# Kernel optimization log

Hardware: AMD Instinct MI355X
Metric: run time of the kernel (lower is better)

The kernel has to match this reference:

```python
import jax, jax.numpy as jnp
import numpy as np

P = 8  # patch size hardcoded in FSAS/DFFN
EPS = 1e-5


def conv1x1(x, w):
    # x: [B,C,H,W], w: [Cout,Cin]
    return jnp.einsum('bchw,oc->bohw', x, w)


def dwconv3(x, w):
    # depthwise 3x3, w: [C,1,3,3]
    return jax.lax.conv_general_dilated(
        x, w, window_strides=(1, 1), padding='SAME',
        dimension_numbers=('NCHW', 'OIHW', 'NCHW'),
        feature_group_count=x.shape[1])


def layernorm_c(x, w, b):
    # WithBias LayerNorm over channel dim (torch: b c h w -> b (h w) c, LN over c)
    mu = jnp.mean(x, axis=1, keepdims=True)
    var = jnp.var(x, axis=1, keepdims=True)
    return (x - mu) / jnp.sqrt(var + EPS) * w[None, :, None, None] + b[None, :, None, None]


def to_patches(x):
    # [B,C,H,W] -> [B,C,H/P,W/P,P,P]
    B, C, H, W = x.shape
    return x.reshape(B, C, H // P, P, W // P, P).transpose(0, 1, 2, 4, 3, 5)


def from_patches(xp):
    B, C, h, w, p1, p2 = xp.shape
    return xp.transpose(0, 1, 2, 4, 3, 5).reshape(B, C, h * p1, w * p2)


def fsas(x, w_hidden, dw, norm_w, norm_b, w_out):
    hidden = conv1x1(x, w_hidden)          # [B,6d,H,W]
    qkv = dwconv3(hidden, dw)
    q, k, v = jnp.split(qkv, 3, axis=1)    # each [B,2d,H,W]
    qf = jnp.fft.rfft2(to_patches(q))
    kf = jnp.fft.rfft2(to_patches(k))
    out = jnp.fft.irfft2(qf * kf, s=(P, P))
    out = layernorm_c(from_patches(out), norm_w, norm_b)
    return conv1x1(v * out, w_out)


def dffn(x, w_in, fft_w, dw, w_out):
    x = conv1x1(x, w_in)                   # [B,2h,H,W]
    xf = jnp.fft.rfft2(to_patches(x))
    # fft_w: [2h,1,1,P,P//2+1] broadcasts against [B,2h,h,w,P,P//2+1]
    x = from_patches(jnp.fft.irfft2(xf * fft_w, s=(P, P)))
    x1, x2 = jnp.split(dwconv3(x, dw), 2, axis=1)
    return conv1x1(jax.nn.gelu(x1, approximate=False) * x2, w_out)


def setup_inputs() -> dict:
    key = jax.random.key(0)
    ks = jax.random.split(key, 10)
    d = 48
    h = int(d * 3)  # ffn_expansion_factor=3 -> hidden_features=144
    B, H, W = 2, 256, 256

    def n(k, shape, s=0.05):
        return jax.random.normal(k, shape, jnp.float32) * s

    return {
        'x': jax.random.normal(ks[0], (B, d, H, W), jnp.float32),
        'norm1_w': jnp.ones((d,), jnp.float32),
        'norm1_b': jnp.zeros((d,), jnp.float32),
        'attn_w_hidden': n(ks[1], (6 * d, d)),
        'attn_dw': n(ks[2], (6 * d, 1, 3, 3), 0.2),
        'attn_norm_w': jnp.ones((2 * d,), jnp.float32),
        'attn_norm_b': jnp.zeros((2 * d,), jnp.float32),
        'attn_w_out': n(ks[3], (d, 2 * d)),
        'norm2_w': jnp.ones((d,), jnp.float32),
        'norm2_b': jnp.zeros((d,), jnp.float32),
        'ffn_w_in': n(ks[4], (2 * h, d)),
        'ffn_fft': 1.0 + n(ks[5], (2 * h, 1, 1, P, P // 2 + 1), 0.1),
        'ffn_dw': n(ks[6], (2 * h, 1, 3, 3), 0.2),
        'ffn_w_out': n(ks[7], (d, h)),
    }


def reference(x, norm1_w, norm1_b, attn_w_hidden, attn_dw, attn_norm_w,
              attn_norm_b, attn_w_out, norm2_w, norm2_b, ffn_w_in, ffn_fft,
              ffn_dw, ffn_w_out):
    x = x + fsas(layernorm_c(x, norm1_w, norm1_b),
                 attn_w_hidden, attn_dw, attn_norm_w, attn_norm_b, attn_w_out)
    x = x + dffn(layernorm_c(x, norm2_w, norm2_b),
                 ffn_w_in, ffn_fft, ffn_dw, ffn_w_out)
    return x
```

## Files before the change

kernel.cpp:

```cpp
#include <hip/hip_runtime.h>
#include <hip/hip_bf16.h>
#include <cstddef>


constexpr int HWC = 65536;

typedef short short8 __attribute__((ext_vector_type(8)));
typedef __bf16 bf16x8 __attribute__((ext_vector_type(8)));
typedef float f32x4 __attribute__((ext_vector_type(4)));
typedef _Float16 f16x8 __attribute__((ext_vector_type(8)));
typedef _Float16 f16x4 __attribute__((ext_vector_type(4)));

__device__ inline unsigned short f2bf(float f) {
  __hip_bfloat16 h = __float2bfloat16(f);
  return *reinterpret_cast<unsigned short*>(&h);
}
__device__ inline float bf2f(unsigned short u) {
  __hip_bfloat16 h;
  *reinterpret_cast<unsigned short*>(&h) = u;
  return __bfloat162float(h);
}

union V8 { uint4 v; unsigned short us[8]; short s[8]; };

__device__ inline void load8f(const unsigned short* p, float* f) {
  V8 u; u.v = *reinterpret_cast<const uint4*>(p);
#pragma unroll
  for (int j = 0; j < 8; j++) f[j] = bf2f(u.us[j]);
}
__device__ inline void store8bf(unsigned short* p, const float* f) {
  V8 u;
#pragma unroll
  for (int j = 0; j < 8; j++) u.us[j] = f2bf(f[j]);
  *reinterpret_cast<uint4*>(p) = u.v;
}

__device__ inline void fdft8(const float* x, float* e) {
  const float c = 0.70710678118654752f;
  float t0 = x[0] + x[4], t1 = x[0] - x[4];
  float t2 = x[2] + x[6], t3 = x[2] - x[6];
  float t4 = x[1] + x[5], t5 = x[1] - x[5];
  float t6 = x[3] + x[7], t7 = x[3] - x[7];
  float A = c * (t5 - t7), B = c * (t5 + t7);
  float s1 = t0 + t2, s2 = t4 + t6;
  e[0] = s1 + s2;
  e[7] = s1 - s2;
  e[1] = t1 + A;
  e[5] = t1 - A;
  e[2] = -(B + t3);
  e[6] = t3 - B;
  e[3] = t0 - t2;
  e[4] = t6 - t4;
}

__device__ inline void idft8(const float* Z, float* acc) {
  const float c2 = 0.70710678118654752f;
  float Z0 = Z[0], Z1r = Z[1], Z1i = Z[2], Z2r = Z[3];
  float Z2i = Z[4], Z3r = Z[5], Z3i = Z[6], Z4 = Z[7];
  float u0 = Z0 + Z4, u1 = Z0 - Z4;
  float E = 2.f * Z2r, F = 2.f * (Z1r + Z3r), G = 2.f * (Z1i - Z3i);
  float T = 2.f * Z2i;
  float P = 2.f * c2 * (Z1r - Z1i), Qv = 2.f * c2 * (Z1r + Z1i);
  float R = 2.f * c2 * (Z3r + Z3i), S = 2.f * c2 * (Z3r - Z3i);
  acc[0] = 0.125f * (u0 + E + F);
  acc[4] = 0.125f * (u0 + E - F);
  acc[2] = 0.125f * (u0 - E - G);
  acc[6] = 0.125f * (u0 - E + G);
  acc[1] = 0.125f * (u1 + P - T - R);
  acc[3] = 0.125f * (u1 - Qv + T + S);
  acc[5] = 0.125f * (u1 - P - T + R);
  acc[7] = 0.125f * (u1 + Qv + T - S);
}

__device__ const float c_cos8[8] = {
    1.f, 0.70710678118654752f, 0.f, -0.70710678118654752f,
    -1.f, -0.70710678118654752f, 0.f, 0.70710678118654752f};

__global__ __launch_bounds__(64) void k_prep_w(
    const float* __restrict__ awh, const float* __restrict__ awo,
    const float* __restrict__ fwi, const float* __restrict__ fwo,
    const float* __restrict__ fftw, unsigned short* __restrict__ wp,
    unsigned short* __restrict__ cmat) {
  __shared__ float sf[64];
  int row = blockIdx.x, t = threadIdx.x;
  if (row >= 672) {
    int c = row - 672;
    int a = t >> 3, b2 = t & 7;
    const float* W = fftw + c * 40;
    float acc = 0.f;
    for (int u = 0; u < 8; u++) {
      for (int v = 0; v < 8; v++) {
        float wv;
        if (v <= 4) {
          if (v == 0 || v == 4)
            wv = 0.5f * (W[u * 5 + v] + W[((8 - u) & 7) * 5 + v]);
          else
            wv = W[u * 5 + v];
        } else {
          wv = W[((8 - u) & 7) * 5 + (8 - v)];
        }
        acc += wv * c_cos8[(u * a + v * b2) & 7];
      }
    }
    sf[t] = acc * (1.f / 64.f);
    __syncthreads();
    unsigned short* cp = cmat + (size_t)c * 4096 + t * 64;
    for (int k8 = 0; k8 < 64; k8 += 8) {
      float v[8];
      int ka = k8 >> 3;
      int ia = ((a - ka) & 7) * 8;
#pragma unroll
      for (int j = 0; j < 8; j++) v[j] = sf[ia + ((b2 - j) & 7)];
      store8bf(cp + k8, v);
    }
    return;
  }
  const float* src; int K, KP; unsigned short* dst;
  if (row < 288)      { src = awh + row * 48;        K = 48;  KP = 64;
                        dst = wp + row * 64; }
  else if (row < 336) { int r = row - 288; src = awo + r * 96; K = 96; KP = 96;
                        dst = wp + 18432 + r * 96; }
  else if (row < 624) { int r = row - 336; src = fwi + r * 48; K = 48; KP = 64;
                        dst = wp + 23040 + r * 64; }
  else                { int r = row - 624; src = fwo + r * 144; K = 144; KP = 160;
                        dst = wp + 41472 + r * 160; }
  for (int k = t; k < KP; k += 64) dst[k] = f2bf(k < K ? src[k] : 0.f);
}

template <int M, int K, int KP, int XF, int EPI>
__global__ __launch_bounds__(256) void k_gemm(
    const unsigned short* __restrict__ wb, const void* __restrict__ s1,
    const unsigned short* __restrict__ s2, const float* __restrict__ lnw,
    const float* __restrict__ lnb, const void* __restrict__ res,
    void* __restrict__ out) {
  constexpr int STRIDE = KP + 8;
  constexpr int KS = KP / 32;
  constexpr int NT = (M + 63) / 64;
  __shared__ __align__(16) short Xs[64 * STRIDE];
  __shared__ __align__(16) short Vs[(XF == 2) ? 64 * STRIDE : 4];
  __shared__ float redS[4][64], redS2[4][64], mus[64], invs[64];

  int tid = threadIdx.x;
  unsigned bid = blockIdx.x;
  int b = (int)(bid >> 10);
  int hw0 = (int)(bid & 1023) * 64;

  if (XF == 1) {
    const float* xp = (const float*)s1 + (size_t)b * 48 * HWC + hw0;
    for (int idx = tid; idx < 48 * 16; idx += 256) {
      int c = idx >> 4, colg = (idx & 15) * 4;
      float4 f = *reinterpret_cast<const float4*>(xp + (size_t)c * HWC + colg);
      Xs[(colg + 0) * STRIDE + c] = (short)f2bf(f.x);
      Xs[(colg + 1) * STRIDE + c] = (short)f2bf(f.y);
      Xs[(colg + 2) * STRIDE + c] = (short)f2bf(f.z);
      Xs[(colg + 3) * STRIDE + c] = (short)f2bf(f.w);
    }
  } else if (XF == 2) {
    const unsigned short* up =
        (const unsigned short*)s1 + (size_t)b * 96 * HWC + hw0;
    const unsigned short* vp = s2 + ((size_t)(b * 288 + 192)) * HWC + hw0;
    for (int idx = tid; idx < 96 * 16; idx += 256) {
      int c = idx >> 4, colg = (idx & 15) * 4;
      ushort4 uv = *reinterpret_cast<const ushort4*>(up + (size_t)c * HWC + colg);
      Xs[(colg + 0) * STRIDE + c] = (short)uv.x;
      Xs[(colg + 1) * STRIDE + c] = (short)uv.y;
      Xs[(colg + 2) * STRIDE + c] = (short)uv.z;
      Xs[(colg + 3) * STRIDE + c] = (short)uv.w;
      ushort4 vv = *reinterpret_cast<const ushort4*>(vp + (size_t)c * HWC + colg);
      Vs[(colg + 0) * STRIDE + c] = (short)vv.x;
      Vs[(colg + 1) * STRIDE + c] = (short)vv.y;
      Vs[(colg + 2) * STRIDE + c] = (short)vv.z;
      Vs[(colg + 3) * STRIDE + c] = (short)vv.w;
    }
  } else if (XF == 3) {
    const unsigned short* xp =
        (const unsigned short*)s1 + (size_t)b * 48 * HWC + hw0;
    for (int idx = tid; idx < 48 * 16; idx += 256) {
      int c = idx >> 4, colg = (idx & 15) * 4;
      ushort4 uv = *reinterpret_cast<const ushort4*>(xp + (size_t)c * HWC + colg);
      Xs[(colg + 0) * STRIDE + c] = (short)uv.x;
      Xs[(colg + 1) * STRIDE + c] = (short)uv.y;
      Xs[(colg + 2) * STRIDE + c] = (short)uv.z;
      Xs[(colg + 3) * STRIDE + c] = (short)uv.w;
    }
  } else {
    const unsigned short* p1 =
        (const unsigned short*)s1 + (size_t)b * 96 * HWC + hw0;
    const unsigned short* p2 = s2 + (size_t)b * 48 * HWC + hw0;
    for (int idx = tid; idx < K * 16; idx += 256) {
      int c = idx >> 4, colg = (idx & 15) * 4;
      const unsigned short* p =
          (c < 96) ? (p1 + (size_t)c * HWC + colg)
                   : (p2 + (size_t)(c - 96) * HWC + colg);
      ushort4 uv = *reinterpret_cast<const ushort4*>(p);
      Xs[(colg + 0) * STRIDE + c] = (short)uv.x;
      Xs[(colg + 1) * STRIDE + c] = (short)uv.y;
      Xs[(colg + 2) * STRIDE + c] = (short)uv.z;
      Xs[(colg + 3) * STRIDE + c] = (short)uv.w;
    }
  }

  if constexpr (KP > K) {
    constexpr int PAD = KP - K;
    for (int idx = tid; idx < 64 * PAD; idx += 256) {
      int col = idx / PAD, c = K + (idx % PAD);
      Xs[col * STRIDE + c] = 0;
    }
  }

  if (XF != 0) {
    constexpr int KC = (XF == 2) ? 96 : 48;
    __syncthreads();
    {
      int col = tid & 63, q = tid >> 6;
      float s = 0.f, s2 = 0.f;
      for (int c = q * (KC / 4); c < (q + 1) * (KC / 4); c++) {
        float v = bf2f((unsigned short)Xs[col * STRIDE + c]);
        s += v; s2 += v * v;
      }
      redS[q][col] = s; redS2[q][col] = s2;
    }
    __syncthreads();
    if (tid < 64) {
      float ss = redS[0][tid] + redS[1][tid] + redS[2][tid] + redS[3][tid];
      float ss2 = redS2[0][tid] + redS2[1][tid] + redS2[2][tid] + redS2[3][tid];
      float mu = ss * (1.f / KC);
      float var = ss2 * (1.f / KC) - mu * mu;
      mus[tid] = mu; invs[tid] = rsqrtf(var + 1e-5f);
    }
    __syncthreads();
    for (int idx = tid; idx < KC * 64; idx += 256) {
      int c = idx >> 6, col = idx & 63;
      float v = bf2f((unsigned short)Xs[col * STRIDE + c]);
      v = (v - mus[col]) * invs[col] * lnw[c] + lnb[c];
      if (XF == 2) v *= bf2f((unsigned short)Vs[col * STRIDE + c]);
      Xs[col * STRIDE + c] = (short)f2bf(v);
    }
  }
  __syncthreads();

  int lane = tid & 63, wvi = tid >> 6;
  int quad = lane >> 4, mc = lane & 15;
  int kbase = quad * 8;

  short8 bfr[4][KS];
#pragma unroll
  for (int ns = 0; ns < 4; ns++)
#pragma unroll
    for (int ks = 0; ks < KS; ks++)
      bfr[ns][ks] = *reinterpret_cast<const short8*>(
          Xs + (ns * 16 + mc) * STRIDE + ks * 32 + kbase);

  short* Es = Xs;
#pragma unroll
  for (int t = 0; t < NT; t++) {
    int mb = (wvi + 4 * t) * 16;
    f32x4 accs[4];
    if (mb < M) {
      short8 afr[KS];
#pragma unroll
      for (int ks = 0; ks < KS; ks++)
        afr[ks] = *reinterpret_cast<const short8*>(
            wb + (size_t)(mb + mc) * KP + ks * 32 + kbase);
#pragma unroll
      for (int ns = 0; ns < 4; ns++) {
        f32x4 acc = {0.f, 0.f, 0.f, 0.f};
#pragma unroll
        for (int ks = 0; ks < KS; ks++)
          acc = __builtin_amdgcn_mfma_f32_16x16x32_bf16(
              __builtin_bit_cast(bf16x8, afr[ks]),
              __builtin_bit_cast(bf16x8, bfr[ns][ks]), acc, 0, 0, 0);
        accs[ns] = acc;
      }
    }
    __syncthreads();
    if (mb < M) {
      int chl = wvi * 16 + quad * 4;
#pragma unroll
      for (int ns = 0; ns < 4; ns++)
#pragma unroll
        for (int r = 0; r < 4; r++)
          Es[(chl + r) * 72 + ns * 16 + mc] = (short)f2bf(accs[ns][r]);
    }
    __syncthreads();
#pragma unroll
    for (int i = 0; i < 2; i++) {
      int chl = (tid >> 3) + 32 * i;
      int px0 = (tid & 7) * 8;
      int m = 64 * t + chl;
      if (m < M) {
        V8 ev;
        ev.v = *reinterpret_cast<const uint4*>(Es + chl * 72 + px0);
        size_t off = ((size_t)(b * ((EPI == 0) ? M : 48) + m)) * HWC + hw0 + px0;
        if (EPI == 0) {
          *reinterpret_cast<uint4*>((unsigned short*)out + off) = ev.v;
        } else if (EPI == 1) {
          const float* rp = (const float*)res + off;
          float4 ra = *reinterpret_cast<const float4*>(rp);
          float4 rb = *reinterpret_cast<const float4*>(rp + 4);
          V8 pk;
          pk.us[0] = f2bf(ra.x + bf2f(ev.us[0]));
          pk.us[1] = f2bf(ra.y + bf2f(ev.us[1]));
          pk.us[2] = f2bf(ra.z + bf2f(ev.us[2]));
          pk.us[3] = f2bf(ra.w + bf2f(ev.us[3]));
          pk.us[4] = f2bf(rb.x + bf2f(ev.us[4]));
          pk.us[5] = f2bf(rb.y + bf2f(ev.us[5]));
          pk.us[6] = f2bf(rb.z + bf2f(ev.us[6]));
          pk.us[7] = f2bf(rb.w + bf2f(ev.us[7]));
          *reinterpret_cast<uint4*>((unsigned short*)out + off) = pk.v;
        } else {
          V8 rv;
          rv.v = *reinterpret_cast<const uint4*>((const unsigned short*)res + off);
          float* op = (float*)out + off;
          float4 oa, ob;
          oa.x = bf2f(rv.us[0]) + bf2f(ev.us[0]);
          oa.y = bf2f(rv.us[1]) + bf2f(ev.us[1]);
          oa.z = bf2f(rv.us[2]) + bf2f(ev.us[2]);
          oa.w = bf2f(rv.us[3]) + bf2f(ev.us[3]);
          ob.x = bf2f(rv.us[4]) + bf2f(ev.us[4]);
          ob.y = bf2f(rv.us[5]) + bf2f(ev.us[5]);
          ob.z = bf2f(rv.us[6]) + bf2f(ev.us[6]);
          ob.w = bf2f(rv.us[7]) + bf2f(ev.us[7]);
          *reinterpret_cast<float4*>(op) = oa;
          *reinterpret_cast<float4*>(op + 4) = ob;
        }
      }
    }
  }
}

__global__ __launch_bounds__(256) void k_fsas_fused(
    const unsigned short* __restrict__ hid, const float* __restrict__ dw,
    unsigned short* __restrict__ out, unsigned short* __restrict__ qkv) {
  constexpr int LSTR = 260;
  __shared__ __align__(16) float qs[8 * LSTR];
  __shared__ __align__(16) float kt[8 * LSTR];
  int tid = threadIdx.x;
  unsigned bid = blockIdx.x;
  int py = (int)(bid & 31);
  unsigned t = bid >> 5;
  int cc = (int)(t % 192u);
  int b = (int)(t / 192u);
  int r = tid >> 5, seg = tid & 31, lane = tid & 63;

  if (cc >= 96) {
    int c = 96 + cc;
    const unsigned short* ip = hid + ((size_t)(b * 288 + c)) * HWC;
    float wv[9];
#pragma unroll
    for (int k = 0; k < 9; k++) wv[k] = dw[c * 9 + k];
    int y = py * 8 + r;
    float f[3][8];
#pragma unroll
    for (int dy = 0; dy < 3; dy++) {
      int yy = y + dy - 1;
      if (yy >= 0 && yy < 256) {
        load8f(ip + yy * 256 + seg * 8, f[dy]);
      } else {
#pragma unroll
        for (int j = 0; j < 8; j++) f[dy][j] = 0.f;
      }
    }
    float o[8];
#pragma unroll
    for (int dy = 0; dy < 3; dy++) {
      float lv = __shfl(f[dy][7], lane - 1, 64);
      float rv = __shfl(f[dy][0], lane + 1, 64);
      if (seg == 0) lv = 0.f;
      if (seg == 31) rv = 0.f;
#pragma unroll
      for (int j = 0; j < 8; j++) {
        float xl = (j == 0) ? lv : f[dy][j - 1];
        float xr = (j == 7) ? rv : f[dy][j + 1];
        float v = xl * wv[dy * 3] + f[dy][j] * wv[dy * 3 + 1] + xr * wv[dy * 3 + 2];
        o[j] = (dy == 0) ? v : o[j] + v;
      }
    }
    store8bf(qkv + ((size_t)(b * 288 + c)) * HWC + y * 256 + seg * 8, o);
    return;
  }

  int c = cc;
  const unsigned short* qp = hid + ((size_t)(b * 288 + c)) * HWC;
  const unsigned short* kp = hid + ((size_t)(b * 288 + 96 + c)) * HWC;
  float w1[9], w2[9];
#pragma unroll
  for (int k = 0; k < 9; k++) {
    w1[k] = dw[c * 9 + k];
    w2[k] = dw[(96 + c) * 9 + k];
  }
  int y = py * 8 + r;
  float f1[3][8], f2[3][8];
#pragma unroll
  for (int dy = 0; dy < 3; dy++) {
    int yy = y + dy - 1;
    if (yy >= 0 && yy < 256) {
      load8f(qp + yy * 256 + seg * 8, f1[dy]);
      load8f(kp + yy * 256 + seg * 8, f2[dy]);
    } else {
#pragma unroll
      for (int j = 0; j < 8; j++) { f1[dy][j] = 0.f; f2[dy][j] = 0.f; }
    }
  }
  float d1[8], d2[8];
#pragma unroll
  for (int j = 0; j < 8; j++) { d1[j] = 0.f; d2[j] = 0.f; }
#pragma unroll
  for (int dy = 0; dy < 3; dy++) {
    float lv1 = __shfl(f1[dy][7], lane - 1, 64);
    float rv1 = __shfl(f1[dy][0], lane + 1, 64);
    float lv2 = __shfl(f2[dy][7], lane - 1, 64);
    float rv2 = __shfl(f2[dy][0], lane + 1, 64);
    if (seg == 0) { lv1 = 0.f; lv2 = 0.f; }
    if (seg == 31) { rv1 = 0.f; rv2 = 0.f; }
#pragma unroll
    for (int j = 0; j < 8; j++) {
      float xl1 = (j == 0) ? lv1 : f1[dy][j - 1];
      float xr1 = (j == 7) ? rv1 : f1[dy][j + 1];
      float xl2 = (j == 0) ? lv2 : f2[dy][j - 1];
      float xr2 = (j == 7) ? rv2 : f2[dy][j + 1];
      d1[j] += xl1 * w1[dy * 3] + f1[dy][j] * w1[dy * 3 + 1] + xr1 * w1[dy * 3 + 2];
      d2[j] += xl2 * w2[dy * 3] + f2[dy][j] * w2[dy * 3 + 1] + xr2 * w2[dy * 3 + 2];
    }
  }
  {
    float e1[8], e2[8];
    fdft8(d1, e1);
    fdft8(d2, e2);
    float4 a1 = {e1[0], e1[1], e1[2], e1[3]};
    float4 b1 = {e1[4], e1[5], e1[6], e1[7]};
    float4 a2 = {e2[0], e2[1], e2[2], e2[3]};
    float4 b2 = {e2[4], e2[5], e2[6], e2[7]};
    *reinterpret_cast<float4*>(&qs[r * LSTR + seg * 8]) = a1;
    *reinterpret_cast<float4*>(&qs[r * LSTR + seg * 8 + 4]) = b1;
    *reinterpret_cast<float4*>(&kt[r * LSTR + seg * 8]) = a2;
    *reinterpret_cast<float4*>(&kt[r * LSTR + seg * 8 + 4]) = b2;
  }
  __syncthreads();
  int p = tid >> 3, a = tid & 7;
  float Z[8];
#pragma unroll
  for (int j = 0; j < 8; j++) Z[j] = 0.f;
#pragma unroll
  for (int i = 0; i < 8; i++) {
    float4 qa = *reinterpret_cast<const float4*>(&qs[i * LSTR + p * 8]);
    float4 qb = *reinterpret_cast<const float4*>(&qs[i * LSTR + p * 8 + 4]);
    int ar = (a - i) & 7;
    float4 ka = *reinterpret_cast<const float4*>(&kt[ar * LSTR + p * 8]);
    float4 kb = *reinterpret_cast<const float4*>(&kt[ar * LSTR + p * 8 + 4]);
    Z[0] += qa.x * ka.x;
    Z[7] += qb.w * kb.w;
    Z[1] += qa.y * ka.y - qa.z * ka.z;
    Z[2] += qa.y * ka.z + qa.z * ka.y;
    Z[3] += qa.w * ka.w - qb.x * kb.x;
    Z[4] += qa.w * kb.x + qb.x * ka.w;
    Z[5] += qb.y * kb.y - qb.z * kb.z;
    Z[6] += qb.y * kb.z + qb.z * kb.y;
  }
  float acc[8];
  idft8(Z, acc);
  store8bf(out + ((size_t)(b * 96 + c)) * HWC + (py * 8 + a) * 256 + p * 8,
           acc);
}

__global__ __launch_bounds__(256) void k_dffn_mfma(
    const unsigned short* __restrict__ y, const unsigned short* __restrict__ cmat,
    const float* __restrict__ dwf, unsigned short* __restrict__ g1,
    unsigned short* __restrict__ g2) {
  constexpr int ZSTR = 264;
  __shared__ __align__(16) short As[64 * 72];
  __shared__ __align__(16) short Bs3[3][32 * 72];
  __shared__ __align__(16) _Float16 zb[2][10 * ZSTR];
  int tid = threadIdx.x;
  unsigned hw = blockIdx.x;
  unsigned bid = (hw & 7u) * 1152u + (hw >> 3);
  int py = (int)(bid & 31);
  int cg = (int)((bid >> 5) % 144u);
  int b  = (int)((bid >> 5) / 144u);
  int y0 = py * 8;
  int lane = tid & 63, wvi = tid >> 6;
  int quad = lane >> 4, mc = lane & 15;
  int kbase = quad * 8;

#pragma unroll
  for (int h = 0; h < 2; h++) {
    int c = cg + h * 144;
    const unsigned short* yp = y + ((size_t)(b * 288 + c)) * HWC;
    __syncthreads();
    {
      const unsigned short* cp = cmat + (size_t)c * 4096;
      int m = tid >> 2, kq = (tid & 3) * 16;
      *reinterpret_cast<uint4*>(As + m * 72 + kq) =
          *reinterpret_cast<const uint4*>(cp + m * 64 + kq);
      *reinterpret_cast<uint4*>(As + m * 72 + kq + 8) =
          *reinterpret_cast<const uint4*>(cp + m * 64 + kq + 8);
    }
    {
      int rr = tid >> 5, seg = tid & 31;
#pragma unroll
      for (int s = 0; s < 3; s++) {
        int slab = py - 1 + s;
        uint4 v = {0u, 0u, 0u, 0u};
        if (slab >= 0 && slab < 32)
          v = *reinterpret_cast<const uint4*>(yp + slab * 2048 + rr * 256 +
                                              seg * 8);
        *reinterpret_cast<uint4*>(&Bs3[s][seg * 72 + rr * 8]) = v;
      }
    }
    __syncthreads();
    {
      short8 afr[2];
#pragma unroll
      for (int ks = 0; ks < 2; ks++)
        afr[ks] = *reinterpret_cast<const short8*>(
            As + (wvi * 16 + mc) * 72 + ks * 32 + kbase);
#pragma unroll
      for (int nt = 0; nt < 2; nt++) {
        f32x4 acc = {0.f, 0.f, 0.f, 0.f};
#pragma unroll
        for (int ks = 0; ks < 2; ks++) {
          short8 bfr = *reinterpret_cast<const short8*>(
              &Bs3[1][(nt * 16 + mc) * 72 + ks * 32 + kbase]);
          acc = __builtin_amdgcn_mfma_f32_16x16x32_bf16(
              __builtin_bit_cast(bf16x8, afr[ks]),
              __builtin_bit_cast(bf16x8, bfr), acc, 0, 0, 0);
        }
        int p = nt * 16 + mc;
        int m0 = wvi * 16 + quad * 4;
        int a = m0 >> 3, b8 = m0 & 7;
        f16x4 z4;
#pragma unroll
        for (int r = 0; r < 4; r++) z4[r] = (_Float16)acc[r];
        *reinterpret_cast<f16x4*>(&zb[h][(1 + a) * ZSTR + p * 8 + b8]) = z4;
      }
    }
    {
      int hb = wvi & 1, nth = wvi >> 1;
      int arow = (hb == 0) ? (56 + (mc & 7)) : (mc & 7);
      const short* Bn = &Bs3[(hb == 0) ? 0 : 2][0];
      f32x4 acc = {0.f, 0.f, 0.f, 0.f};
#pragma unroll
      for (int ks = 0; ks < 2; ks++) {
        short8 afr = *reinterpret_cast<const short8*>(
            As + arow * 72 + ks * 32 + kbase);
        short8 bfr = *reinterpret_cast<const short8*>(
            Bn + (nth * 16 + mc) * 72 + ks * 32 + kbase);
        acc = __builtin_amdgcn_mfma_f32_16x16x32_bf16(
            __builtin_bit_cast(bf16x8, afr),
            __builtin_bit_cast(bf16x8, bfr), acc, 0, 0, 0);
      }
      if (quad < 2) {
        int p = nth * 16 + mc;
        int m0 = quad * 4;
        f16x4 z4;
#pragma unroll
        for (int r = 0; r < 4; r++) z4[r] = (_Float16)acc[r];
        *reinterpret_cast<f16x4*>(
            &zb[h][(hb ? 9 : 0) * ZSTR + p * 8 + m0]) = z4;
      }
    }
  }
  __syncthreads();
  int r = tid >> 5, seg = tid & 31;
  float w1[9], w2[9];
#pragma unroll
  for (int k = 0; k < 9; k++) {
    w1[k] = dwf[cg * 9 + k];
    w2[k] = dwf[(144 + cg) * 9 + k];
  }
  float d1[8], d2[8];
#pragma unroll
  for (int j = 0; j < 8; j++) { d1[j] = 0.f; d2[j] = 0.f; }
#pragma unroll
  for (int dy = 0; dy < 3; dy++) {
    int zr = r + dy;
    {
      const _Float16* z = &zb[0][zr * ZSTR];
      f16x8 cv = *reinterpret_cast<const f16x8*>(&z[seg * 8]);
      float lv = (seg == 0) ? 0.f : (float)z[seg * 8 - 1];
      float rv = (seg == 31) ? 0.f : (float)z[seg * 8 + 8];
#pragma unroll
      for (int j = 0; j < 8; j++) {
        float xl = (j == 0) ? lv : (float)cv[j - 1];
        float xr = (j == 7) ? rv : (float)cv[j + 1];
        d1[j] += xl * w1[dy * 3] + (float)cv[j] * w1[dy * 3 + 1] + xr * w1[dy * 3 + 2];
      }
    }
    {
      const _Float16* z = &zb[1][zr * ZSTR];
      f16x8 cv = *reinterpret_cast<const f16x8*>(&z[seg * 8]);
      float lv = (seg == 0) ? 0.f : (float)z[seg * 8 - 1];
      float rv = (seg == 31) ? 0.f : (float)z[seg * 8 + 8];
#pragma unroll
      for (int j = 0; j < 8; j++) {
        float xl = (j == 0) ? lv : (float)cv[j - 1];
        float xr = (j == 7) ? rv : (float)cv[j + 1];
        d2[j] += xl * w2[dy * 3] + (float)cv[j] * w2[dy * 3 + 1] + xr * w2[dy * 3 + 2];
      }
    }
  }
  float o[8];
#pragma unroll
  for (int j = 0; j < 8; j++)
    o[j] = 0.5f * d1[j] * (1.f + erff(d1[j] * 0.70710678118654752f)) * d2[j];
  unsigned short* gp = (cg < 96)
      ? g1 + ((size_t)(b * 96 + cg)) * HWC
      : g2 + ((size_t)(b * 48 + (cg - 96))) * HWC;
  store8bf(gp + (y0 + r) * 256 + seg * 8, o);
}

extern "C" void kernel_launch(void* const* d_in, const int* in_sizes, int n_in,
                              void* d_out, int out_size, void* d_ws,
                              size_t ws_size, hipStream_t stream) {
  (void)in_sizes; (void)n_in; (void)out_size; (void)ws_size;
  const float* x   = (const float*)d_in[0];
  const float* n1w = (const float*)d_in[1];
  const float* n1b = (const float*)d_in[2];
  const float* awh = (const float*)d_in[3];
  const float* adw = (const float*)d_in[4];
  const float* anw = (const float*)d_in[5];
  const float* anb = (const float*)d_in[6];
  const float* awo = (const float*)d_in[7];
  const float* n2w = (const float*)d_in[8];
  const float* n2b = (const float*)d_in[9];
  const float* fwi = (const float*)d_in[10];
  const float* fff = (const float*)d_in[11];
  const float* fdw = (const float*)d_in[12];
  const float* fwo = (const float*)d_in[13];

  unsigned short* QKV  = (unsigned short*)d_ws;
  unsigned short* HID  = (unsigned short*)((char*)d_ws + 75497472);
  unsigned short* U    = (unsigned short*)((char*)d_ws + 150994944);
  unsigned short* X1   = (unsigned short*)((char*)d_ws + 176160768);
  unsigned short* G2   = (unsigned short*)((char*)d_ws + 188743680);
  unsigned short* WP   = (unsigned short*)((char*)d_ws + 201326592);
  unsigned short* CMAT = (unsigned short*)((char*)d_ws + 201424896);
  unsigned short* WA = WP;
  unsigned short* WO = WP + 18432;
  unsigned short* WI = WP + 23040;
  unsigned short* WF = WP + 41472;

  k_prep_w<<<960, 64, 0, stream>>>(awh, awo, fwi, fwo, fff, WP, CMAT);
  k_gemm<288, 48, 64, 1, 0><<<2048, 256, 0, stream>>>(WA, x, nullptr, n1w,
                                                      n1b, nullptr, HID);
  k_fsas_fused<<<2 * 192 * 32, 256, 0, stream>>>(HID, adw, U, QKV);
  k_gemm<48, 96, 96, 2, 1><<<2048, 256, 0, stream>>>(WO, U, QKV, anw, anb, x,
                                                     X1);
  k_gemm<288, 48, 64, 3, 0><<<2048, 256, 0, stream>>>(WI, X1, nullptr, n2w,
                                                      n2b, nullptr, QKV);
  k_dffn_mfma<<<2 * 144 * 32, 256, 0, stream>>>(QKV, CMAT, fdw, U, G2);
  k_gemm<48, 144, 160, 0, 2><<<2048, 256, 0, stream>>>(WF, U, G2, nullptr,
                                                       nullptr, X1,
                                                       (float*)d_out);
}
```

Baseline: 280.2 us.

## Fuse attention output projection with LayerNorm2 and FFN input projection

Combines the attention output GEMM (with its LayerNorm and v-gating), the residual add, LayerNorm2 and the FFN input GEMM into one kernel. The 48-channel intermediate stays in shared memory per 64-pixel tile, so the second GEMM no longer re-reads X1 from global memory, and one launch is saved. X1 is still written out because the final GEMM needs it as its residual. The fused kernel uses more shared memory and more barriers, which may lower occupancy. It also reads and writes the QKV buffer in the same kernel; this is safe only because each block touches its own pixel columns.

```diff
diff --git a/kernel.cpp b/kernel.cpp
--- a/kernel.cpp
+++ b/kernel.cpp
@@ -137,7 +137,6 @@
   constexpr int KS = KP / 32;
   constexpr int NT = (M + 63) / 64;
   __shared__ __align__(16) short Xs[64 * STRIDE];
-  __shared__ __align__(16) short Vs[(XF == 2) ? 64 * STRIDE : 4];
   __shared__ float redS[4][64], redS2[4][64], mus[64], invs[64];
 
   int tid = threadIdx.x;
@@ -154,34 +153,6 @@
       Xs[(colg + 1) * STRIDE + c] = (short)f2bf(f.y);
       Xs[(colg + 2) * STRIDE + c] = (short)f2bf(f.z);
       Xs[(colg + 3) * STRIDE + c] = (short)f2bf(f.w);
-    }
-  } else if (XF == 2) {
-    const unsigned short* up =
-        (const unsigned short*)s1 + (size_t)b * 96 * HWC + hw0;
-    const unsigned short* vp = s2 + ((size_t)(b * 288 + 192)) * HWC + hw0;
-    for (int idx = tid; idx < 96 * 16; idx += 256) {
-      int c = idx >> 4, colg = (idx & 15) * 4;
-      ushort4 uv = *reinterpret_cast<const ushort4*>(up + (size_t)c * HWC + colg);
-      Xs[(colg + 0) * STRIDE + c] = (short)uv.x;
-      Xs[(colg + 1) * STRIDE + c] = (short)uv.y;
-      Xs[(colg + 2) * STRIDE + c] = (short)uv.z;
-      Xs[(colg + 3) * STRIDE + c] = (short)uv.w;
-      ushort4 vv = *reinterpret_cast<const ushort4*>(vp + (size_t)c * HWC + colg);
-      Vs[(colg + 0) * STRIDE + c] = (short)vv.x;
-      Vs[(colg + 1) * STRIDE + c] = (short)vv.y;
-      Vs[(colg + 2) * STRIDE + c] = (short)vv.z;
-      Vs[(colg + 3) * STRIDE + c] = (short)vv.w;
-    }
-  } else if (XF == 3) {
-    const unsigned short* xp =
-        (const unsigned short*)s1 + (size_t)b * 48 * HWC + hw0;
-    for (int idx = tid; idx < 48 * 16; idx += 256) {
-      int c = idx >> 4, colg = (idx & 15) * 4;
-      ushort4 uv = *reinterpret_cast<const ushort4*>(xp + (size_t)c * HWC + colg);
-      Xs[(colg + 0) * STRIDE + c] = (short)uv.x;
-      Xs[(colg + 1) * STRIDE + c] = (short)uv.y;
-      Xs[(colg + 2) * STRIDE + c] = (short)uv.z;
-      Xs[(colg + 3) * STRIDE + c] = (short)uv.w;
     }
   } else {
     const unsigned short* p1 =
@@ -208,8 +179,8 @@
     }
   }
 
-  if (XF != 0) {
-    constexpr int KC = (XF == 2) ? 96 : 48;
+  if (XF == 1) {
+    constexpr int KC = 48;
     __syncthreads();
     {
       int col = tid & 63, q = tid >> 6;
@@ -233,7 +204,6 @@
       int c = idx >> 6, col = idx & 63;
       float v = bf2f((unsigned short)Xs[col * STRIDE + c]);
       v = (v - mus[col]) * invs[col] * lnw[c] + lnb[c];
-      if (XF == 2) v *= bf2f((unsigned short)Vs[col * STRIDE + c]);
       Xs[col * STRIDE + c] = (short)f2bf(v);
     }
   }
@@ -294,20 +264,6 @@
         size_t off = ((size_t)(b * ((EPI == 0) ? M : 48) + m)) * HWC + hw0 + px0;
         if (EPI == 0) {
           *reinterpret_cast<uint4*>((unsigned short*)out + off) = ev.v;
-        } else if (EPI == 1) {
-          const float* rp = (const float*)res + off;
-          float4 ra = *reinterpret_cast<const float4*>(rp);
-          float4 rb = *reinterpret_cast<const float4*>(rp + 4);
-          V8 pk;
-          pk.us[0] = f2bf(ra.x + bf2f(ev.us[0]));
-          pk.us[1] = f2bf(ra.y + bf2f(ev.us[1]));
-          pk.us[2] = f2bf(ra.z + bf2f(ev.us[2]));
-          pk.us[3] = f2bf(ra.w + bf2f(ev.us[3]));
-          pk.us[4] = f2bf(rb.x + bf2f(ev.us[4]));
-          pk.us[5] = f2bf(rb.y + bf2f(ev.us[5]));
-          pk.us[6] = f2bf(rb.z + bf2f(ev.us[6]));
-          pk.us[7] = f2bf(rb.w + bf2f(ev.us[7]));
-          *reinterpret_cast<uint4*>((unsigned short*)out + off) = pk.v;
         } else {
           V8 rv;
           rv.v = *reinterpret_cast<const uint4*>((const unsigned short*)res + off);
@@ -324,6 +280,207 @@
           *reinterpret_cast<float4*>(op) = oa;
           *reinterpret_cast<float4*>(op + 4) = ob;
         }
+      }
+    }
+  }
+}
+
+__global__ __launch_bounds__(256) void k_gemm23(
+    const unsigned short* __restrict__ wo, const unsigned short* __restrict__ wi,
+    const unsigned short* __restrict__ u, unsigned short* __restrict__ qkv,
+    const float* __restrict__ anw, const float* __restrict__ anb,
+    const float* __restrict__ n2w, const float* __restrict__ n2b,
+    const float* __restrict__ x, unsigned short* __restrict__ x1) {
+  constexpr int S1 = 104;
+  constexpr int S2 = 72;
+  __shared__ __align__(16) short Xs[64 * S1];
+  __shared__ __align__(16) short Vs[64 * S1];
+  __shared__ float redS[4][64], redS2[4][64], mus[64], invs[64];
+
+  int tid = threadIdx.x;
+  unsigned bid = blockIdx.x;
+  int b = (int)(bid >> 10);
+  int hw0 = (int)(bid & 1023) * 64;
+
+  {
+    const unsigned short* up = u + (size_t)b * 96 * HWC + hw0;
+    const unsigned short* vp = qkv + ((size_t)(b * 288 + 192)) * HWC + hw0;
+    for (int idx = tid; idx < 96 * 16; idx += 256) {
+      int c = idx >> 4, colg = (idx & 15) * 4;
+      ushort4 uv = *reinterpret_cast<const ushort4*>(up + (size_t)c * HWC + colg);
+      Xs[(colg + 0) * S1 + c] = (short)uv.x;
+      Xs[(colg + 1) * S1 + c] = (short)uv.y;
+      Xs[(colg + 2) * S1 + c] = (short)uv.z;
+      Xs[(colg + 3) * S1 + c] = (short)uv.w;
+      ushort4 vv = *reinterpret_cast<const ushort4*>(vp + (size_t)c * HWC + colg);
+      Vs[(colg + 0) * S1 + c] = (short)vv.x;
+      Vs[(colg + 1) * S1 + c] = (short)vv.y;
+      Vs[(colg + 2) * S1 + c] = (short)vv.z;
+      Vs[(colg + 3) * S1 + c] = (short)vv.w;
+    }
+  }
+  __syncthreads();
+  {
+    int col = tid & 63, q = tid >> 6;
+    float s = 0.f, s2 = 0.f;
+    for (int c = q * 24; c < (q + 1) * 24; c++) {
+      float v = bf2f((unsigned short)Xs[col * S1 + c]);
+      s += v; s2 += v * v;
+    }
+    redS[q][col] = s; redS2[q][col] = s2;
+  }
+  __syncthreads();
+  if (tid < 64) {
+    float ss = redS[0][tid] + redS[1][tid] + redS[2][tid] + redS[3][tid];
+    float ss2 = redS2[0][tid] + redS2[1][tid] + redS2[2][tid] + redS2[3][tid];
+    float mu = ss * (1.f / 96.f);
+    float var = ss2 * (1.f / 96.f) - mu * mu;
+    mus[tid] = mu; invs[tid] = rsqrtf(var + 1e-5f);
+  }
+  __syncthreads();
+  for (int idx = tid; idx < 96 * 64; idx += 256) {
+    int c = idx >> 6, col = idx & 63;
+    float v = bf2f((unsigned short)Xs[col * S1 + c]);
+    v = (v - mus[col]) * invs[col] * anw[c] + anb[c];
+    v *= bf2f((unsigned short)Vs[col * S1 + c]);
+    Xs[col * S1 + c] = (short)f2bf(v);
+  }
+  __syncthreads();
+
+  int lane = tid & 63, wvi = tid >> 6;
+  int quad = lane >> 4, mc = lane & 15;
+  int kbase = quad * 8;
+
+  short8 bfr1[4][3];
+#pragma unroll
+  for (int ns = 0; ns < 4; ns++)
+#pragma unroll
+    for (int ks = 0; ks < 3; ks++)
+      bfr1[ns][ks] = *reinterpret_cast<const short8*>(
+          Xs + (ns * 16 + mc) * S1 + ks * 32 + kbase);
+  bool act1 = (wvi < 3);
+  f32x4 acc1[4];
+  if (act1) {
+    int mb = wvi * 16;
+    short8 afr[3];
+#pragma unroll
+    for (int ks = 0; ks < 3; ks++)
+      afr[ks] = *reinterpret_cast<const short8*>(
+          wo + (size_t)(mb + mc) * 96 + ks * 32 + kbase);
+#pragma unroll
+    for (int ns = 0; ns < 4; ns++) {
+      f32x4 acc = {0.f, 0.f, 0.f, 0.f};
+#pragma unroll
+      for (int ks = 0; ks < 3; ks++)
+        acc = __builtin_amdgcn_mfma_f32_16x16x32_bf16(
+            __builtin_bit_cast(bf16x8, afr[ks]),
+            __builtin_bit_cast(bf16x8, bfr1[ns][ks]), acc, 0, 0, 0);
+      acc1[ns] = acc;
+    }
+  }
+  __syncthreads();
+  if (act1) {
+    int chl = wvi * 16 + quad * 4;
+#pragma unroll
+    for (int ns = 0; ns < 4; ns++) {
+      int px = ns * 16 + mc;
+#pragma unroll
+      for (int r = 0; r < 4; r++) {
+        int m = chl + r;
+        float xr = x[((size_t)(b * 48 + m)) * HWC + hw0 + px];
+        Vs[px * S2 + m] = (short)f2bf(acc1[ns][r] + xr);
+      }
+    }
+  }
+  for (int idx = tid; idx < 64 * 16; idx += 256) {
+    int col = idx >> 4, c = 48 + (idx & 15);
+    Vs[col * S2 + c] = 0;
+  }
+  __syncthreads();
+  for (int u2 = tid; u2 < 48 * 8; u2 += 256) {
+    int m = u2 >> 3, px0 = (u2 & 7) * 8;
+    V8 pk;
+#pragma unroll
+    for (int j = 0; j < 8; j++)
+      pk.us[j] = (unsigned short)Vs[(px0 + j) * S2 + m];
+    *reinterpret_cast<uint4*>(x1 + ((size_t)(b * 48 + m)) * HWC + hw0 + px0) =
+        pk.v;
+  }
+  {
+    int col = tid & 63, q = tid >> 6;
+    float s = 0.f, s2 = 0.f;
+    for (int c = q * 12; c < (q + 1) * 12; c++) {
+      float v = bf2f((unsigned short)Vs[col * S2 + c]);
+      s += v; s2 += v * v;
+    }
+    redS[q][col] = s; redS2[q][col] = s2;
+  }
+  __syncthreads();
+  if (tid < 64) {
+    float ss = redS[0][tid] + redS[1][tid] + redS[2][tid] + redS[3][tid];
+    float ss2 = redS2[0][tid] + redS2[1][tid] + redS2[2][tid] + redS2[3][tid];
+    float mu = ss * (1.f / 48.f);
+    float var = ss2 * (1.f / 48.f) - mu * mu;
+    mus[tid] = mu; invs[tid] = rsqrtf(var + 1e-5f);
+  }
+  __syncthreads();
+  for (int idx = tid; idx < 48 * 64; idx += 256) {
+    int c = idx >> 6, col = idx & 63;
+    float v = bf2f((unsigned short)Vs[col * S2 + c]);
+    v = (v - mus[col]) * invs[col] * n2w[c] + n2b[c];
+    Vs[col * S2 + c] = (short)f2bf(v);
+  }
+  __syncthreads();
+
+  short8 bfr2[4][2];
+#pragma unroll
+  for (int ns = 0; ns < 4; ns++)
+#pragma unroll
+    for (int ks = 0; ks < 2; ks++)
+      bfr2[ns][ks] = *reinterpret_cast<const short8*>(
+          Vs + (ns * 16 + mc) * S2 + ks * 32 + kbase);
+  short* Es = Xs;
+#pragma unroll
+  for (int t = 0; t < 5; t++) {
+    int mb = (wvi + 4 * t) * 16;
+    f32x4 accs[4];
+    if (mb < 288) {
+      short8 afr[2];
+#pragma unroll
+      for (int ks = 0; ks < 2; ks++)
+        afr[ks] = *reinterpret_cast<const short8*>(
+            wi + (size_t)(mb + mc) * 64 + ks * 32 + kbase);
+#pragma unroll
+      for (int ns = 0; ns < 4; ns++) {
+        f32x4 acc = {0.f, 0.f, 0.f, 0.f};
+#pragma unroll
+        for (int ks = 0; ks < 2; ks++)
+          acc = __builtin_amdgcn_mfma_f32_16x16x32_bf16(
+              __builtin_bit_cast(bf16x8, afr[ks]),
+              __builtin_bit_cast(bf16x8, bfr2[ns][ks]), acc, 0, 0, 0);
+        accs[ns] = acc;
+      }
+    }
+    __syncthreads();
+    if (mb < 288) {
+      int chl = wvi * 16 + quad * 4;
+#pragma unroll
+      for (int ns = 0; ns < 4; ns++)
+#pragma unroll
+        for (int r = 0; r < 4; r++)
+          Es[(chl + r) * 72 + ns * 16 + mc] = (short)f2bf(accs[ns][r]);
+    }
+    __syncthreads();
+#pragma unroll
+    for (int i = 0; i < 2; i++) {
+      int chl = (tid >> 3) + 32 * i;
+      int px0 = (tid & 7) * 8;
+      int m = 64 * t + chl;
+      if (m < 288) {
+        V8 ev;
+        ev.v = *reinterpret_cast<const uint4*>(Es + chl * 72 + px0);
+        *reinterpret_cast<uint4*>(
+            qkv + ((size_t)(b * 288 + m)) * HWC + hw0 + px0) = ev.v;
       }
     }
   }
@@ -644,10 +801,8 @@
   k_gemm<288, 48, 64, 1, 0><<<2048, 256, 0, stream>>>(WA, x, nullptr, n1w,
                                                       n1b, nullptr, HID);
   k_fsas_fused<<<2 * 192 * 32, 256, 0, stream>>>(HID, adw, U, QKV);
-  k_gemm<48, 96, 96, 2, 1><<<2048, 256, 0, stream>>>(WO, U, QKV, anw, anb, x,
-                                                     X1);
-  k_gemm<288, 48, 64, 3, 0><<<2048, 256, 0, stream>>>(WI, X1, nullptr, n2w,
-                                                      n2b, nullptr, QKV);
+  k_gemm23<<<2048, 256, 0, stream>>>(WO, WI, U, QKV, anw, anb, n2w, n2b, x,
+                                     X1);
   k_dffn_mfma<<<2 * 144 * 32, 256, 0, stream>>>(QKV, CMAT, fdw, U, G2);
   k_gemm<48, 144, 160, 0, 2><<<2048, 256, 0, stream>>>(WF, U, G2, nullptr,
                                                        nullptr, X1,
```

Result: faster. 272.3 us (-2.8%).
